# Optimization experiments

Hardware: AMD Instinct MI355X
Metric: run time of the kernel (lower is better)

Reference implementation:

```python
import jax, jax.numpy as jnp
import numpy as np

NUM_SLOTS = 64
MEMORY_DIM = 512
EMBED_DIM = 1024
SCALE = MEMORY_DIM ** (-0.5)


def setup_inputs() -> dict:
    key = jax.random.key(0)
    ks = jax.random.split(key, 7)
    B, S, E, Dm = 8, 4096, EMBED_DIM, MEMORY_DIM
    s = 0.02
    return {
        "embeddings": jax.random.normal(ks[0], (B, S, E), dtype=jnp.float32),
        "W_write": jax.random.normal(ks[1], (E, Dm), dtype=jnp.float32) * s,
        "b_write": jnp.zeros((Dm,), dtype=jnp.float32),
        "W_query": jax.random.normal(ks[2], (E, Dm), dtype=jnp.float32) * s,
        "b_query": jnp.zeros((Dm,), dtype=jnp.float32),
        "W_out": jax.random.normal(ks[3], (Dm, E), dtype=jnp.float32) * s,
        "b_out": jnp.zeros((E,), dtype=jnp.float32),
    }


def reference(embeddings, W_write, b_write, W_query, b_query, W_out, b_out):
    B, S, E = embeddings.shape
    M, Dm = NUM_SLOTS, MEMORY_DIM
    # Precompute per-token projections (linear, so identical to per-step).
    write_vals = jnp.einsum('bse,ed->bsd', embeddings, W_write) + b_write  # [B,S,Dm]
    queries = jnp.einsum('bse,ed->bsd', embeddings, W_query) + b_query      # [B,S,Dm]
    addrs = jnp.arange(S) % M  # hash(position) = position % M

    def step(carry, xs):
        memory, written = carry            # [B,M,Dm], [B,M] bool
        q, wv, addr = xs                   # [B,Dm], [B,Dm], scalar int
        # read BEFORE write (current token not yet in memory)
        sim = jnp.einsum('bd,bmd->bm', q, memory) * SCALE
        sim = jnp.where(written, sim, -jnp.inf)
        attn = jax.nn.softmax(sim, axis=-1)
        attn = jnp.nan_to_num(attn)        # all-unwritten -> zeros
        retrieved = jnp.einsum('bm,bmd->bd', attn, memory)
        memory = memory.at[:, addr, :].set(wv)
        written = written.at[:, addr].set(True)
        return (memory, written), retrieved

    mem0 = jnp.zeros((B, M, Dm), dtype=embeddings.dtype)
    wr0 = jnp.zeros((B, M), dtype=bool)
    xs = (queries.transpose(1, 0, 2), write_vals.transpose(1, 0, 2), addrs)
    _, retrieved = jax.lax.scan(step, (mem0, wr0), xs)  # [S,B,Dm]
    retrieved = retrieved.transpose(1, 0, 2)            # [B,S,Dm]
    # read_out is linear per-step -> apply once over the whole sequence
    return jnp.einsum('bsd,de->bse', retrieved, W_out) + b_out
```

## Files before the change

kernel.cpp:

```cpp
#include <hip/hip_runtime.h>
#include <hip/hip_bf16.h>
#include <math.h>


#define BATCH   8
#define S_LEN   4096
#define EMB     1024
#define DM      512
#define MROWS   (BATCH * S_LEN)
#define SCALE_F 0.04419417382415922f

typedef __attribute__((ext_vector_type(4))) float f32x4;
typedef __attribute__((ext_vector_type(8))) short short8;

__device__ __forceinline__ unsigned short f2bf(float f) {
    __hip_bfloat16 h = __float2bfloat16(f);
    return *reinterpret_cast<unsigned short*>(&h);
}

__global__ __launch_bounds__(256) void cast_bf16(const float4* __restrict__ in,
                                                 ushort4* __restrict__ out, int n4)
{
    int id = blockIdx.x * 256 + threadIdx.x;
    if (id >= n4) return;
    float4 v = in[id];
    ushort4 o;
    o.x = f2bf(v.x); o.y = f2bf(v.y); o.z = f2bf(v.z); o.w = f2bf(v.w);
    out[id] = o;
}

__global__ __launch_bounds__(256) void tcast(const float* __restrict__ in,
                                             __hip_bfloat16* __restrict__ out,
                                             int K, int N)
{
    int id = blockIdx.x * 256 + threadIdx.x;
    if (id >= K * N) return;
    int n = id / K, k = id % K;
    out[id] = __float2bfloat16(in[k * N + n]);
}

__global__ __launch_bounds__(256) void concat_bias(const float* __restrict__ a,
                                                   const float* __restrict__ b,
                                                   float* __restrict__ out)
{
    int i = blockIdx.x * 256 + threadIdx.x;
    if (i < 512) out[i] = a[i];
    else if (i < 1024) out[i] = b[i - 512];
}

template<bool BF16OUT>
__global__ __launch_bounds__(512, 2) void gemm256(
    const __hip_bfloat16* __restrict__ A, int lda,
    const __hip_bfloat16* __restrict__ Bt, int ldb,
    const float* __restrict__ bias,
    void* __restrict__ Cv, int ldc,
    int K, int nbx)
{
    __shared__ __align__(16) char smem[131072];

    const int nwg = gridDim.x;
    const int bid = blockIdx.x;
    const int cpx = nwg >> 3;
    const int swz = (bid & 7) * cpx + (bid >> 3);
    const int bm0 = (swz / nbx) << 8;
    const int bn0 = (swz % nbx) << 8;

    const int tid  = threadIdx.x;
    const int lane = tid & 63;
    const int w    = tid >> 6;
    const int wm   = w >> 2, wn = w & 3;
    const int l15  = lane & 15, lhi = lane >> 4;
    const int nt   = K >> 6;

    const int srow  = w * 8 + (lane >> 3);
    const int scol8 = (((lane & 7) ^ (lane >> 3)) << 3);

    auto stage_tile = [&](int buf, int kt) {
#pragma unroll
        for (int h = 0; h < 4; ++h) {
            const int isB = h >> 1, hh = h & 1;
            const __hip_bfloat16* G = isB ? Bt : A;
            const int ldg = isB ? ldb : lda;
            const int rb  = (isB ? bn0 : bm0) + hh * 128;
#pragma unroll
            for (int i = 0; i < 2; ++i) {
                const __hip_bfloat16* g =
                    G + (size_t)(rb + i * 64 + srow) * ldg + kt + scol8;
                char* l = smem + buf * 65536 + isB * 32768 + hh * 16384
                          + i * 8192 + w * 1024;
                __builtin_amdgcn_global_load_lds(
                    (const __attribute__((address_space(1))) unsigned int*)g,
                    (__attribute__((address_space(3))) unsigned int*)l, 16, 0, 0);
            }
        }
    };

    f32x4 acc[8][4] = {};

    stage_tile(0, 0);
    __syncthreads();

    for (int t = 0; t < nt; ++t) {
        const int cur = t & 1;
        if (t + 1 < nt) stage_tile(cur ^ 1, (t + 1) << 6);

        const char* sA = smem + cur * 65536;
        const char* sB = sA + 32768;

#pragma unroll
        for (int q = 0; q < 4; ++q) {
            const int mh = q >> 1, nh = q & 1;
            short8 af[4][2], bfv[2][2];
#pragma unroll
            for (int mi = 0; mi < 4; ++mi) {
                const int r = wm * 128 + mh * 64 + mi * 16 + l15;
#pragma unroll
                for (int kk = 0; kk < 2; ++kk) {
                    const int pc = (kk * 4 + lhi) ^ (r & 7);
                    af[mi][kk] = *(const short8*)(sA + r * 128 + (pc << 4));
                }
            }
#pragma unroll
            for (int ni = 0; ni < 2; ++ni) {
                const int r = wn * 64 + nh * 32 + ni * 16 + l15;
#pragma unroll
                for (int kk = 0; kk < 2; ++kk) {
                    const int pc = (kk * 4 + lhi) ^ (r & 7);
                    bfv[ni][kk] = *(const short8*)(sB + r * 128 + (pc << 4));
                }
            }
#pragma unroll
            for (int mi = 0; mi < 4; ++mi)
#pragma unroll
                for (int ni = 0; ni < 2; ++ni)
#pragma unroll
                    for (int kk = 0; kk < 2; ++kk)
                        acc[mh * 4 + mi][nh * 2 + ni] =
                            __builtin_amdgcn_mfma_f32_16x16x32_bf16(
                                af[mi][kk], bfv[ni][kk],
                                acc[mh * 4 + mi][nh * 2 + ni], 0, 0, 0);
        }
        __syncthreads();
    }

    float bv[4];
#pragma unroll
    for (int N = 0; N < 4; ++N)
        bv[N] = bias[bn0 + wn * 64 + (N >> 1) * 32 + (N & 1) * 16 + l15];

#pragma unroll
    for (int M = 0; M < 8; ++M)
#pragma unroll
        for (int N = 0; N < 4; ++N)
#pragma unroll
            for (int reg = 0; reg < 4; ++reg) {
                int row = bm0 + wm * 128 + (M >> 2) * 64 + (M & 3) * 16
                          + lhi * 4 + reg;
                int col = bn0 + wn * 64 + (N >> 1) * 32 + (N & 1) * 16 + l15;
                float v = acc[M][N][reg] + bv[N];
                if (BF16OUT)
                    ((__hip_bfloat16*)Cv)[(size_t)row * ldc + col] = __float2bfloat16(v);
                else
                    ((float*)Cv)[(size_t)row * ldc + col] = v;
            }
}

__global__ __launch_bounds__(256) void transpose_wv(
    const unsigned short* __restrict__ wvq,
    unsigned short* __restrict__ wvt)
{
    __shared__ unsigned short tl[64][66];
    const int tx  = blockIdx.x;
    const int dx  = blockIdx.y;
    const int b   = blockIdx.z;
    const int tid = threadIdx.x;
    const int r   = tid >> 3;
    const int c8  = (tid & 7) * 8;
    const size_t bbase = (size_t)b << 12;

#pragma unroll
    for (int it = 0; it < 2; ++it) {
        int row = r + it * 32;
        uint4 v = *(const uint4*)(wvq + ((bbase + tx * 64 + row) << 10) + dx * 64 + c8);
        *(unsigned*)&tl[row][c8 + 0] = v.x;
        *(unsigned*)&tl[row][c8 + 2] = v.y;
        *(unsigned*)&tl[row][c8 + 4] = v.z;
        *(unsigned*)&tl[row][c8 + 6] = v.w;
    }
    __syncthreads();
#pragma unroll
    for (int it = 0; it < 2; ++it) {
        int drow = r + it * 32;
        union { unsigned short s[8]; uint4 v; } o;
#pragma unroll
        for (int k = 0; k < 8; ++k) o.s[k] = tl[c8 + k][drow];
        *(uint4*)(wvt + (((size_t)b * 512 + dx * 64 + drow) << 12) + tx * 64 + c8) = o.v;
    }
}

__global__ __launch_bounds__(256) void attn_mfma(
    const __hip_bfloat16* __restrict__ WVQ,
    const __hip_bfloat16* __restrict__ WVT,
    __hip_bfloat16* __restrict__ R)
{
    __shared__ __align__(16) unsigned short p_lds[64][136];

    const int blk = blockIdx.x;
    const int b   = blk >> 6;
    const int t0  = (blk & 63) << 6;
    const int jmin = (t0 == 0) ? 64 : 0;
    const size_t bbase = (size_t)b << 12;
    const int tid  = threadIdx.x;
    const int lane = tid & 63;
    const int w    = tid >> 6;
    const int l15  = lane & 15;
    const int lhi  = lane >> 4;

    f32x4 acc[8] = {};
    const __hip_bfloat16* q0 =
        WVQ + ((bbase + t0 + w * 16 + l15) << 10) + 512 + lhi * 8;

    const __hip_bfloat16* brow[8];
#pragma unroll
    for (int nt = 0; nt < 8; ++nt) {
        int aj = t0 - 64 + nt * 16 + l15;
        if (aj < 0) aj = 0;
        brow[nt] = WVQ + ((bbase + aj) << 10) + lhi * 8;
    }

    for (int kt = 0; kt < 16; ++kt) {
        short8 qa = *(const short8*)(q0 + kt * 32);
#pragma unroll
        for (int nt = 0; nt < 8; ++nt) {
            short8 bv = *(const short8*)(brow[nt] + kt * 32);
            acc[nt] = __builtin_amdgcn_mfma_f32_16x16x32_bf16(qa, bv, acc[nt], 0, 0, 0);
        }
    }

    float m4[4] = { -1e30f, -1e30f, -1e30f, -1e30f };
#pragma unroll
    for (int nt = 0; nt < 8; ++nt)
#pragma unroll
        for (int reg = 0; reg < 4; ++reg) {
            int i = w * 16 + lhi * 4 + reg;
            int j = nt * 16 + l15;
            bool valid = (j >= i) && (j <= i + 63) && (j >= jmin);
            float s = valid ? acc[nt][reg] * SCALE_F : -1e30f;
            acc[nt][reg] = s;
            m4[reg] = fmaxf(m4[reg], s);
        }
#pragma unroll
    for (int off = 8; off >= 1; off >>= 1)
#pragma unroll
        for (int reg = 0; reg < 4; ++reg)
            m4[reg] = fmaxf(m4[reg], __shfl_xor(m4[reg], off, 64));

    float sum4[4] = {};
#pragma unroll
    for (int nt = 0; nt < 8; ++nt)
#pragma unroll
        for (int reg = 0; reg < 4; ++reg) {
            float s = acc[nt][reg];
            float p = (s > -1e29f) ? __expf(s - m4[reg]) : 0.f;
            acc[nt][reg] = p;
            sum4[reg] += p;
        }
#pragma unroll
    for (int off = 8; off >= 1; off >>= 1)
#pragma unroll
        for (int reg = 0; reg < 4; ++reg)
            sum4[reg] += __shfl_xor(sum4[reg], off, 64);

    float rs4[4];
#pragma unroll
    for (int reg = 0; reg < 4; ++reg)
        rs4[reg] = (sum4[reg] > 0.f) ? 1.f / sum4[reg] : 0.f;

#pragma unroll
    for (int nt = 0; nt < 8; ++nt)
#pragma unroll
        for (int reg = 0; reg < 4; ++reg)
            p_lds[w * 16 + lhi * 4 + reg][nt * 16 + l15] =
                f2bf(acc[nt][reg] * rs4[reg]);

    __syncthreads();

    short8 pa[4];
#pragma unroll
    for (int kt = 0; kt < 4; ++kt)
        pa[kt] = *(const short8*)&p_lds[w * 16 + l15][kt * 32 + lhi * 8];

    int tclamp[4];
#pragma unroll
    for (int kt = 0; kt < 4; ++kt) {
        int ti = t0 - 64 + kt * 32 + lhi * 8;
        tclamp[kt] = ti < 0 ? 0 : ti;
    }

    const size_t vbase = (size_t)b * 512;
    for (int nt = 0; nt < 32; ++nt) {
        int d = nt * 16 + l15;
        f32x4 a = {};
#pragma unroll
        for (int kt = 0; kt < 4; ++kt) {
            short8 bv = *(const short8*)(WVT + ((vbase + d) << 12) + tclamp[kt]);
            a = __builtin_amdgcn_mfma_f32_16x16x32_bf16(pa[kt], bv, a, 0, 0, 0);
        }
        size_t rb = (bbase + t0 + w * 16 + lhi * 4) << 9;
#pragma unroll
        for (int reg = 0; reg < 4; ++reg)
            R[rb + ((size_t)reg << 9) + d] = __float2bfloat16(a[reg]);
    }
}

extern "C" void kernel_launch(void* const* d_in, const int* in_sizes, int n_in,
                              void* d_out, int out_size, void* d_ws, size_t ws_size,
                              hipStream_t stream)
{
    const float* emb   = (const float*)d_in[0];
    const float* W_wr  = (const float*)d_in[1];
    const float* b_wr  = (const float*)d_in[2];
    const float* W_qr  = (const float*)d_in[3];
    const float* b_qr  = (const float*)d_in[4];
    const float* W_out = (const float*)d_in[5];
    const float* b_out = (const float*)d_in[6];
    float* out = (float*)d_out;

    char* ws = (char*)d_ws;
    __hip_bfloat16* embb = (__hip_bfloat16*)(ws);
    __hip_bfloat16* wvt  = (__hip_bfloat16*)(ws);
    __hip_bfloat16* wvq  = (__hip_bfloat16*)(ws + (((size_t)64) << 20));
    __hip_bfloat16* rbuf = (__hip_bfloat16*)(ws + (((size_t)128) << 20));
    __hip_bfloat16* wcat = (__hip_bfloat16*)(ws + (((size_t)160) << 20));
    __hip_bfloat16* wout = (__hip_bfloat16*)(ws + (((size_t)162) << 20));
    float*          bcat = (float*)        (ws + (((size_t)163) << 20));

    cast_bf16<<<dim3((MROWS * EMB / 4) / 256), dim3(256), 0, stream>>>(
        (const float4*)emb, (ushort4*)embb, MROWS * EMB / 4);
    tcast<<<dim3(2048), dim3(256), 0, stream>>>(W_wr, wcat, EMB, DM);
    tcast<<<dim3(2048), dim3(256), 0, stream>>>(W_qr, wcat + (size_t)DM * EMB, EMB, DM);
    tcast<<<dim3(2048), dim3(256), 0, stream>>>(W_out, wout, DM, EMB);
    concat_bias<<<dim3(4), dim3(256), 0, stream>>>(b_wr, b_qr, bcat);

    gemm256<true><<<dim3(512), dim3(512), 0, stream>>>(
        embb, EMB, wcat, EMB, bcat, (void*)wvq, 1024, EMB, 4);

    transpose_wv<<<dim3(64, 8, 8), dim3(256), 0, stream>>>(
        (const unsigned short*)wvq, (unsigned short*)wvt);

    attn_mfma<<<dim3(MROWS / 64), dim3(256), 0, stream>>>(wvq, wvt, rbuf);

    gemm256<false><<<dim3(512), dim3(512), 0, stream>>>(
        rbuf, DM, wout, DM, b_out, (void*)out, EMB, DM, 4);
}
```

Before: 250.6 us.

## Fuse fp32-to-bf16 embedding cast into projection GEMM A-tile loading

Removes the standalone cast kernel that converted the 128MB fp32 embedding tensor to bf16. The projection GEMM now loads fp32 A tiles into registers, converts them, and writes bf16 into LDS after the MFMA loop, prefetching one tile ahead. This drops a full read and write pass over the embeddings. In exchange the first GEMM reads twice as many A bytes, uses more registers, and loses the async global-to-LDS path for A.

New measurement: 242.1 us. -3.4%, faster.

```diff
diff --git a/kernel.cpp b/kernel.cpp
--- a/kernel.cpp
+++ b/kernel.cpp
@@ -18,17 +18,6 @@
     return *reinterpret_cast<unsigned short*>(&h);
 }
 
-__global__ __launch_bounds__(256) void cast_bf16(const float4* __restrict__ in,
-                                                 ushort4* __restrict__ out, int n4)
-{
-    int id = blockIdx.x * 256 + threadIdx.x;
-    if (id >= n4) return;
-    float4 v = in[id];
-    ushort4 o;
-    o.x = f2bf(v.x); o.y = f2bf(v.y); o.z = f2bf(v.z); o.w = f2bf(v.w);
-    out[id] = o;
-}
-
 __global__ __launch_bounds__(256) void tcast(const float* __restrict__ in,
                                              __hip_bfloat16* __restrict__ out,
                                              int K, int N)
@@ -48,9 +37,9 @@
     else if (i < 1024) out[i] = b[i - 512];
 }
 
-template<bool BF16OUT>
+template<bool BF16OUT, bool AF32>
 __global__ __launch_bounds__(512, 2) void gemm256(
-    const __hip_bfloat16* __restrict__ A, int lda,
+    const void* __restrict__ Av, int lda,
     const __hip_bfloat16* __restrict__ Bt, int ldb,
     const float* __restrict__ bias,
     void* __restrict__ Cv, int ldc,
@@ -72,37 +61,82 @@
     const int l15  = lane & 15, lhi = lane >> 4;
     const int nt   = K >> 6;
 
-    const int srow  = w * 8 + (lane >> 3);
-    const int scol8 = (((lane & 7) ^ (lane >> 3)) << 3);
-
-    auto stage_tile = [&](int buf, int kt) {
-#pragma unroll
-        for (int h = 0; h < 4; ++h) {
-            const int isB = h >> 1, hh = h & 1;
-            const __hip_bfloat16* G = isB ? Bt : A;
-            const int ldg = isB ? ldb : lda;
-            const int rb  = (isB ? bn0 : bm0) + hh * 128;
+    const int r64 = tid >> 3;
+    const int cg8 = ((tid & 7) ^ (r64 & 7)) << 3;
+
+    const __hip_bfloat16* Ab = (const __hip_bfloat16*)Av;
+    const float*          Af = (const float*)Av;
+
+    auto stageB = [&](int buf, int kt) {
+#pragma unroll
+        for (int hh = 0; hh < 2; ++hh)
 #pragma unroll
             for (int i = 0; i < 2; ++i) {
                 const __hip_bfloat16* g =
-                    G + (size_t)(rb + i * 64 + srow) * ldg + kt + scol8;
-                char* l = smem + buf * 65536 + isB * 32768 + hh * 16384
-                          + i * 8192 + w * 1024;
+                    Bt + (size_t)(bn0 + hh * 128 + i * 64 + r64) * ldb + kt + cg8;
+                char* l = smem + buf * 65536 + 32768 + hh * 16384 + i * 8192
+                          + w * 1024;
                 __builtin_amdgcn_global_load_lds(
                     (const __attribute__((address_space(1))) unsigned int*)g,
                     (__attribute__((address_space(3))) unsigned int*)l, 16, 0, 0);
             }
-        }
     };
+    auto stageA_lds = [&](int buf, int kt) {
+#pragma unroll
+        for (int hh = 0; hh < 2; ++hh)
+#pragma unroll
+            for (int i = 0; i < 2; ++i) {
+                const __hip_bfloat16* g =
+                    Ab + (size_t)(bm0 + hh * 128 + i * 64 + r64) * lda + kt + cg8;
+                char* l = smem + buf * 65536 + hh * 16384 + i * 8192 + w * 1024;
+                __builtin_amdgcn_global_load_lds(
+                    (const __attribute__((address_space(1))) unsigned int*)g,
+                    (__attribute__((address_space(3))) unsigned int*)l, 16, 0, 0);
+            }
+    };
+
+    float4 areg[4][2];
+    auto loadA = [&](int kt) {
+#pragma unroll
+        for (int p = 0; p < 4; ++p) {
+            const int hh = p >> 1, i = p & 1;
+            const float* g = Af + (size_t)(bm0 + hh * 128 + i * 64 + r64) * lda
+                             + kt + cg8;
+            areg[p][0] = *(const float4*)g;
+            areg[p][1] = *(const float4*)(g + 4);
+        }
+    };
+    auto writeA = [&](int buf) {
+#pragma unroll
+        for (int p = 0; p < 4; ++p) {
+            const int hh = p >> 1, i = p & 1;
+            union { unsigned short s[8]; short8 v; } o;
+            const float* f0 = (const float*)&areg[p][0];
+            const float* f1 = (const float*)&areg[p][1];
+#pragma unroll
+            for (int k2 = 0; k2 < 4; ++k2) {
+                o.s[k2]     = f2bf(f0[k2]);
+                o.s[4 + k2] = f2bf(f1[k2]);
+            }
+            *(short8*)(smem + buf * 65536 + hh * 16384 + i * 8192 + tid * 16) = o.v;
+        }
+    };
 
     f32x4 acc[8][4] = {};
 
-    stage_tile(0, 0);
+    stageB(0, 0);
+    if (AF32) { loadA(0); writeA(0); }
+    else      { stageA_lds(0, 0); }
     __syncthreads();
 
     for (int t = 0; t < nt; ++t) {
         const int cur = t & 1;
-        if (t + 1 < nt) stage_tile(cur ^ 1, (t + 1) << 6);
+        const bool pf = (t + 1 < nt);
+        if (pf) {
+            stageB(cur ^ 1, (t + 1) << 6);
+            if (AF32) loadA((t + 1) << 6);
+            else      stageA_lds(cur ^ 1, (t + 1) << 6);
+        }
 
         const char* sA = smem + cur * 65536;
         const char* sB = sA + 32768;
@@ -140,6 +174,8 @@
                                 af[mi][kk], bfv[ni][kk],
                                 acc[mh * 4 + mi][nh * 2 + ni], 0, 0, 0);
         }
+
+        if (AF32 && pf) writeA(cur ^ 1);
         __syncthreads();
     }
 
@@ -327,7 +363,6 @@
     float* out = (float*)d_out;
 
     char* ws = (char*)d_ws;
-    __hip_bfloat16* embb = (__hip_bfloat16*)(ws);
     __hip_bfloat16* wvt  = (__hip_bfloat16*)(ws);
     __hip_bfloat16* wvq  = (__hip_bfloat16*)(ws + (((size_t)64) << 20));
     __hip_bfloat16* rbuf = (__hip_bfloat16*)(ws + (((size_t)128) << 20));
@@ -335,21 +370,19 @@
     __hip_bfloat16* wout = (__hip_bfloat16*)(ws + (((size_t)162) << 20));
     float*          bcat = (float*)        (ws + (((size_t)163) << 20));
 
-    cast_bf16<<<dim3((MROWS * EMB / 4) / 256), dim3(256), 0, stream>>>(
-        (const float4*)emb, (ushort4*)embb, MROWS * EMB / 4);
     tcast<<<dim3(2048), dim3(256), 0, stream>>>(W_wr, wcat, EMB, DM);
     tcast<<<dim3(2048), dim3(256), 0, stream>>>(W_qr, wcat + (size_t)DM * EMB, EMB, DM);
     tcast<<<dim3(2048), dim3(256), 0, stream>>>(W_out, wout, DM, EMB);
     concat_bias<<<dim3(4), dim3(256), 0, stream>>>(b_wr, b_qr, bcat);
 
-    gemm256<true><<<dim3(512), dim3(512), 0, stream>>>(
-        embb, EMB, wcat, EMB, bcat, (void*)wvq, 1024, EMB, 4);
+    gemm256<true, true><<<dim3(512), dim3(512), 0, stream>>>(
+        (const void*)emb, EMB, wcat, EMB, bcat, (void*)wvq, 1024, EMB, 4);
 
     transpose_wv<<<dim3(64, 8, 8), dim3(256), 0, stream>>>(
         (const unsigned short*)wvq, (unsigned short*)wvt);
 
     attn_mfma<<<dim3(MROWS / 64), dim3(256), 0, stream>>>(wvq, wvt, rbuf);
 
-    gemm256<false><<<dim3(512), dim3(512), 0, stream>>>(
-        rbuf, DM, wout, DM, b_out, (void*)out, EMB, DM, 4);
-}
+    gemm256<false, false><<<dim3(512), dim3(512), 0, stream>>>(
+        (const void*)rbuf, DM, wout, DM, b_out, (void*)out, EMB, DM, 4);
+}
```
